# Optimization experiments

Hardware: AMD Instinct MI355X
Metric: run time of the kernel (lower is better)

The kernel has to match this reference:

```python
import jax, jax.numpy as jnp
import numpy as np

IN_CHANNELS = 128
N_NODES = 100000
N_EDGES = 625000


def setup_inputs() -> dict:
    key = jax.random.key(0)
    k1, k2, k3, k4, k5, k6 = jax.random.split(key, 6)
    d = IN_CHANNELS
    x = jax.random.normal(k1, (N_NODES, d), dtype=jnp.float32)
    edge_index = jax.random.randint(k2, (2, N_EDGES), 0, N_NODES, dtype=jnp.int64)
    # Linear params, torch default init: U(-1/sqrt(fan_in), 1/sqrt(fan_in))
    b1_bound = 1.0 / np.sqrt(2 * d)
    W1 = jax.random.uniform(k3, (d, 2 * d), minval=-b1_bound, maxval=b1_bound, dtype=jnp.float32)
    b1 = jax.random.uniform(k4, (d,), minval=-b1_bound, maxval=b1_bound, dtype=jnp.float32)
    b2_bound = 1.0 / np.sqrt(d)
    W2 = jax.random.uniform(k5, (1, d), minval=-b2_bound, maxval=b2_bound, dtype=jnp.float32)
    b2 = jax.random.uniform(k6, (1,), minval=-b2_bound, maxval=b2_bound, dtype=jnp.float32)
    return {"x": x, "edge_index": edge_index, "W1": W1, "b1": b1, "W2": W2, "b2": b2}


def reference(x, edge_index, W1, b1, W2, b2):
    # Gather endpoint features and concat along feature dim: [E, 2d]
    h = jnp.concatenate([x[edge_index[0]], x[edge_index[1]]], axis=1)
    h = jax.nn.relu(h @ W1.T + b1)          # [E, d]
    h = jax.nn.relu(h @ W2.T + b2)          # [E, 1]
    return jax.nn.sigmoid(h)
```

## Files before the change

kernel.cpp:

```cpp
#include <hip/hip_runtime.h>
#include <hip/hip_bf16.h>
#include <hip/hip_fp16.h>
#include <math.h>


typedef short    s16x4 __attribute__((ext_vector_type(4)));
typedef short    s16x8 __attribute__((ext_vector_type(8)));
typedef float    f32x4 __attribute__((ext_vector_type(4)));
typedef _Float16 h16x2 __attribute__((ext_vector_type(2)));
typedef _Float16 h16x8 __attribute__((ext_vector_type(8)));

#define D    128
#define CWLD 80

static __device__ inline short f2bf(float f) {
    unsigned u = __builtin_bit_cast(unsigned, f);
    unsigned r = (u + 0x7FFFu + ((u >> 16) & 1u)) >> 16;
    return (short)r;
}

static __device__ inline unsigned enc1_sw(float f) {
    f = fminf(fmaxf(f, -448.f), 448.f);
    unsigned short h = __builtin_bit_cast(unsigned short, (_Float16)(f * (1.0f / 256.0f)));
    unsigned s = (h >> 8) & 0x80u;
    unsigned mag = h & 0x7FFFu;
    mag = mag + 0x3Fu + ((mag >> 7) & 1u);
    return s | ((mag >> 7) & 0x7Fu);
}
static __device__ inline unsigned enc2(float a, float b) {
#if __has_builtin(__builtin_amdgcn_cvt_pk_fp8_f32)
    return ((unsigned)__builtin_amdgcn_cvt_pk_fp8_f32(a, b, 0, false)) & 0xFFFFu;
#else
    return enc1_sw(a) | (enc1_sw(b) << 8);
#endif
}

#if __has_builtin(__builtin_amdgcn_cvt_pk_f16_fp8)
#define YSC 1.0f
static __device__ inline h16x2 dec2lo(unsigned v) {
    return __builtin_amdgcn_cvt_pk_f16_fp8((short)v);
}
static __device__ inline h16x2 dec2hi(unsigned v) {
    return __builtin_amdgcn_cvt_pk_f16_fp8((short)(v >> 16));
}
#else
#define YSC 256.0f
static __device__ inline h16x2 dec2lo(unsigned v) {
    unsigned p = __builtin_amdgcn_perm(0u, v, 0x0C010C00u);
    unsigned h = ((p << 8) & 0x80008000u) | ((p << 7) & 0x3F803F80u);
    return __builtin_bit_cast(h16x2, h);
}
static __device__ inline h16x2 dec2hi(unsigned v) {
    unsigned p = __builtin_amdgcn_perm(0u, v, 0x0C030C02u);
    unsigned h = ((p << 8) & 0x80008000u) | ((p << 7) & 0x3F803F80u);
    return __builtin_bit_cast(h16x2, h);
}
#endif

static __device__ inline h16x2 reluh(h16x2 v) {
#if __has_builtin(__builtin_elementwise_max)
    h16x2 z = { (_Float16)0.0f, (_Float16)0.0f };
    return __builtin_elementwise_max(v, z);
#else
    unsigned u = __builtin_bit_cast(unsigned, v);
    unsigned m = ((u >> 15) & 0x00010001u) * 0xFFFFu;
    u &= ~m;
    return __builtin_bit_cast(h16x2, u);
#endif
}

static __device__ inline float dot2acc(h16x2 a, h16x2 b, float c) {
#if __has_builtin(__builtin_amdgcn_fdot2)
    return __builtin_amdgcn_fdot2(a, b, c, false);
#else
    return c + (float)a[0] * (float)b[0] + (float)a[1] * (float)b[1];
#endif
}

__global__ __launch_bounds__(256) void pack_w1_kernel(
    const float* __restrict__ W1, short* __restrict__ W1F)
{
    int g    = blockIdx.x * 256 + threadIdx.x;
    int lane = g & 63;
    int c    = (g >> 6) & 3;
    int j    = (g >> 8) & 3;
    int cs   = g >> 10;
    int o    = cs * 64 + j * 16 + (lane & 15);
    int kb   = c * 32 + (lane >> 4) * 8;
    const float* wp = W1 + (size_t)(o & 127) * 256 + (o >> 7) * 128 + kb;
    float4 u0 = *(const float4*)wp;
    float4 u1 = *(const float4*)(wp + 4);
    s16x8 v = { f2bf(u0.x), f2bf(u0.y), f2bf(u0.z), f2bf(u0.w),
                f2bf(u1.x), f2bf(u1.y), f2bf(u1.z), f2bf(u1.w) };
    *(s16x8*)&W1F[(size_t)g * 8] = v;
}

__global__ __launch_bounds__(64) void precompute_kernel(
    const float* __restrict__ x,
    const short* __restrict__ W1F,
    const float* __restrict__ b1,
    unsigned char* __restrict__ Y8,
    int N)
{
    __shared__ _Float16 Cw[32 * CWLD];

    const int lane = threadIdx.x;
    const int quad = lane >> 4, l15 = lane & 15;
    const int cs   = blockIdx.x;
    const int m0   = blockIdx.y * 32;

    float4 ar[2][4][2];
    #pragma unroll
    for (int i = 0; i < 2; ++i) {
        int m = m0 + i * 16 + l15; if (m >= N) m = N - 1;
        const float* xp = &x[(size_t)m * D + quad * 8];
        #pragma unroll
        for (int c = 0; c < 4; ++c) {
            ar[i][c][0] = *(const float4*)(xp + c * 32);
            ar[i][c][1] = *(const float4*)(xp + c * 32 + 4);
        }
    }

    s16x8 bf[4][4];
    #pragma unroll
    for (int j = 0; j < 4; ++j)
        #pragma unroll
        for (int c = 0; c < 4; ++c)
            bf[c][j] = *(const s16x8*)&W1F[(size_t)(((cs * 4 + j) * 4 + c) * 64 + lane) * 8];

    f32x4 acc[2][4] = {};
    #pragma unroll
    for (int c = 0; c < 4; ++c) {
        s16x8 af[2];
        #pragma unroll
        for (int i = 0; i < 2; ++i)
            af[i] = (s16x8){ f2bf(ar[i][c][0].x), f2bf(ar[i][c][0].y),
                             f2bf(ar[i][c][0].z), f2bf(ar[i][c][0].w),
                             f2bf(ar[i][c][1].x), f2bf(ar[i][c][1].y),
                             f2bf(ar[i][c][1].z), f2bf(ar[i][c][1].w) };
        #pragma unroll
        for (int i = 0; i < 2; ++i)
            #pragma unroll
            for (int j = 0; j < 4; ++j)
                acc[i][j] = __builtin_amdgcn_mfma_f32_16x16x32_bf16(
                    af[i], bf[c][j], acc[i][j], 0, 0, 0);
    }

    float b1v[4];
    #pragma unroll
    for (int j = 0; j < 4; ++j)
        b1v[j] = (cs < 2) ? b1[cs * 64 + j * 16 + l15] : 0.f;

    #pragma unroll
    for (int i = 0; i < 2; ++i)
        #pragma unroll
        for (int j = 0; j < 4; ++j)
            #pragma unroll
            for (int r = 0; r < 4; ++r)
                Cw[(i * 16 + quad * 4 + r) * CWLD + j * 16 + l15] =
                    (_Float16)(acc[i][j][r] + b1v[j]);

    __syncthreads();

    #pragma unroll
    for (int p = 0; p < 2; ++p) {
        int row = p * 16 + (lane >> 2);
        int m   = m0 + row;
        if (m < N) {
            const _Float16* sp = &Cw[row * CWLD + (lane & 3) * 16];
            uint4 ov;
            unsigned dw[4];
            #pragma unroll
            for (int q = 0; q < 4; ++q)
                dw[q] = enc2((float)sp[q*4+0], (float)sp[q*4+1])
                      | (enc2((float)sp[q*4+2], (float)sp[q*4+3]) << 16);
            ov.x = dw[0]; ov.y = dw[1]; ov.z = dw[2]; ov.w = dw[3];
            *(uint4*)&Y8[(size_t)m * 256 + cs * 64 + (lane & 3) * 16] = ov;
        }
    }
}

#define EPB 128

__global__ __launch_bounds__(256) void edge_kernel(
    const unsigned char* __restrict__ Y8,
    const int*           __restrict__ ei,
    const float*         __restrict__ W2,
    const float*         __restrict__ b2,
    float*               __restrict__ out,
    int E)
{
    const int tid = threadIdx.x;
    const int sub = tid & 7;
    const int grp = tid >> 3;
    const int e0  = blockIdx.x * EPB + grp;

    h16x2 w2h[8];
    {
        const float* wp = &W2[sub * 16];
        #pragma unroll
        for (int q = 0; q < 8; ++q) {
            float2 f = *(const float2*)(wp + q * 2);
            w2h[q] = (h16x2){ (_Float16)(f.x * YSC), (_Float16)(f.y * YSC) };
        }
    }

    int  ee[4]; bool vv[4]; uint4 L[4], R[4];
    #pragma unroll
    for (int k = 0; k < 4; ++k) {
        ee[k] = e0 + 32 * k;
        vv[k] = (ee[k] < E);
        int src = vv[k] ? ei[ee[k]] : 0;
        int dst = vv[k] ? ei[E + ee[k]] : 0;
        L[k] = *(const uint4*)(Y8 + (size_t)src * 256 + sub * 16);
        R[k] = *(const uint4*)(Y8 + (size_t)dst * 256 + 128 + sub * 16);
    }

    float s[4] = { 0.f, 0.f, 0.f, 0.f };
    #pragma unroll
    for (int k = 0; k < 4; ++k) {
        const unsigned* a = (const unsigned*)&L[k];
        const unsigned* c = (const unsigned*)&R[k];
        #pragma unroll
        for (int d = 0; d < 4; ++d) {
            h16x2 za = reluh(dec2lo(a[d]) + dec2lo(c[d]));
            s[k] = dot2acc(za, w2h[2*d],     s[k]);
            h16x2 zb = reluh(dec2hi(a[d]) + dec2hi(c[d]));
            s[k] = dot2acc(zb, w2h[2*d + 1], s[k]);
        }
    }

    #pragma unroll
    for (int k = 0; k < 4; ++k) {
        s[k] += __shfl_xor(s[k], 1);
        s[k] += __shfl_xor(s[k], 2);
        s[k] += __shfl_xor(s[k], 4);
    }

    if (sub == 0) {
        float bb = b2[0];
        #pragma unroll
        for (int k = 0; k < 4; ++k) {
            if (vv[k]) {
                float t = fmaxf(s[k] + bb, 0.f);
                out[ee[k]] = 1.0f / (1.0f + expf(-t));
            }
        }
    }
}

#define BM   128
#define BK   64
#define LDT  72

__global__ __launch_bounds__(256) void decoder_fallback_kernel(
    const float* __restrict__ x, const int* __restrict__ ei,
    const float* __restrict__ W1, const float* __restrict__ b1,
    const float* __restrict__ W2, const float* __restrict__ b2,
    float* __restrict__ out, int E)
{
    __shared__ int   nid[2][BM];
    __shared__ short At[BM * LDT];
    __shared__ short Bt[D * LDT];
    __shared__ float rowsum[BM][2];

    const int tid = threadIdx.x;
    const int e0  = blockIdx.x * BM;
    if (tid < BM) { int e = e0 + tid; nid[0][tid] = (e < E) ? ei[e] : 0; }
    else { int e = e0 + (tid - BM); nid[1][tid - BM] = (e < E) ? ei[E + e] : 0; }

    const int wid = tid >> 6, lane = tid & 63;
    const int wm = wid >> 1, wn = wid & 1;
    const int quad = lane >> 4, l15 = lane & 15;
    const int srow = tid >> 4, scol = (tid & 15) * 4;
    f32x4 acc[4][4] = {};
    __syncthreads();

    for (int t = 0; t < 4; ++t) {
        const int* ids = nid[t >> 1];
        const int kx = (t & 1) * BK, kw = t * BK;
        #pragma unroll
        for (int p = 0; p < 8; ++p) {
            int row = srow + p * 16;
            float4 v = *(const float4*)&x[(size_t)ids[row] * D + kx + scol];
            s16x4 bv = { f2bf(v.x), f2bf(v.y), f2bf(v.z), f2bf(v.w) };
            *(s16x4*)&At[row * LDT + scol] = bv;
        }
        #pragma unroll
        for (int p = 0; p < 8; ++p) {
            int n = srow + p * 16;
            float4 v = *(const float4*)&W1[n * 256 + kw + scol];
            s16x4 bv = { f2bf(v.x), f2bf(v.y), f2bf(v.z), f2bf(v.w) };
            *(s16x4*)&Bt[n * LDT + scol] = bv;
        }
        __syncthreads();
        #pragma unroll
        for (int c = 0; c < 2; ++c) {
            const int kc = c * 32;
            s16x8 af[4], bfr[4];
            #pragma unroll
            for (int i = 0; i < 4; ++i)
                af[i] = *(const s16x8*)&At[(wm*64 + i*16 + l15) * LDT + kc + quad*8];
            #pragma unroll
            for (int j = 0; j < 4; ++j)
                bfr[j] = *(const s16x8*)&Bt[(wn*64 + j*16 + l15) * LDT + kc + quad*8];
            #pragma unroll
            for (int i = 0; i < 4; ++i)
                #pragma unroll
                for (int j = 0; j < 4; ++j)
                    acc[i][j] = __builtin_amdgcn_mfma_f32_16x16x32_bf16(
                        af[i], bfr[j], acc[i][j], 0, 0, 0);
        }
        __syncthreads();
    }
    float b1v[4], w2v[4];
    #pragma unroll
    for (int j = 0; j < 4; ++j) {
        int col = wn*64 + j*16 + l15;
        b1v[j] = b1[col]; w2v[j] = W2[col];
    }
    float psum[16];
    #pragma unroll
    for (int t = 0; t < 16; ++t) psum[t] = 0.f;
    #pragma unroll
    for (int i = 0; i < 4; ++i)
        #pragma unroll
        for (int j = 0; j < 4; ++j)
            #pragma unroll
            for (int r = 0; r < 4; ++r) {
                float c = fmaxf(acc[i][j][r] + b1v[j], 0.f);
                psum[i*4 + r] += c * w2v[j];
            }
    #pragma unroll
    for (int off = 1; off < 16; off <<= 1)
        #pragma unroll
        for (int t = 0; t < 16; ++t)
            psum[t] += __shfl_xor(psum[t], off);
    if (l15 == 0) {
        #pragma unroll
        for (int i = 0; i < 4; ++i)
            #pragma unroll
            for (int r = 0; r < 4; ++r)
                rowsum[wm*64 + i*16 + quad*4 + r][wn] = psum[i*4 + r];
    }
    __syncthreads();
    if (tid < BM) {
        int e = e0 + tid;
        if (e < E) {
            float s = rowsum[tid][0] + rowsum[tid][1] + b2[0];
            s = fmaxf(s, 0.f);
            out[e] = 1.0f / (1.0f + expf(-s));
        }
    }
}

extern "C" void kernel_launch(void* const* d_in, const int* in_sizes, int n_in,
                              void* d_out, int out_size, void* d_ws, size_t ws_size,
                              hipStream_t stream) {
    const float* x  = (const float*)d_in[0];
    const int*   ei = (const int*)d_in[1];
    const float* W1 = (const float*)d_in[2];
    const float* b1 = (const float*)d_in[3];
    const float* W2 = (const float*)d_in[4];
    const float* b2 = (const float*)d_in[5];
    float* out = (float*)d_out;

    int E = in_sizes[1] / 2;
    int N = in_sizes[0] / D;

    size_t y_bytes = (size_t)N * 256;
    size_t need    = y_bytes + 32768 * sizeof(short);
    if (ws_size >= need) {
        unsigned char* Y8  = (unsigned char*)d_ws;
        short*         W1F = (short*)((char*)d_ws + y_bytes);
        pack_w1_kernel<<<16, 256, 0, stream>>>(W1, W1F);
        dim3 gridA(4, (N + 31) / 32);
        precompute_kernel<<<gridA, 64, 0, stream>>>(x, W1F, b1, Y8, N);
        int gridB = (E + EPB - 1) / EPB;
        edge_kernel<<<gridB, 256, 0, stream>>>(Y8, ei, W2, b2, out, E);
    } else {
        int nblocks = (E + BM - 1) / BM;
        decoder_fallback_kernel<<<nblocks, 256, 0, stream>>>(
            x, ei, W1, b1, W2, b2, out, E);
    }
}
```

Baseline: 151.8 us.

## Share x tile across four column-slice waves via LDS in precompute kernel

The precompute kernel now launches one 256-thread block per 32-row tile, with four waves each handling one 64-column output slice. Previously four separate 64-thread blocks each loaded and converted the same x rows. The x tile is loaded once cooperatively, converted to bf16 into shared memory, and read back as MFMA A-fragments. This cuts redundant global reads of x and repeated f32-to-bf16 conversion by four times, at the cost of an extra barrier, more LDS per block and fewer blocks.

```diff
diff --git a/kernel.cpp b/kernel.cpp
--- a/kernel.cpp
+++ b/kernel.cpp
@@ -11,6 +11,7 @@
 typedef _Float16 h16x8 __attribute__((ext_vector_type(8)));
 
 #define D    128
+#define ALD  136
 #define CWLD 80
 
 static __device__ inline short f2bf(float f) {
@@ -95,30 +96,32 @@
     *(s16x8*)&W1F[(size_t)g * 8] = v;
 }
 
-__global__ __launch_bounds__(64) void precompute_kernel(
+__global__ __launch_bounds__(256) void precompute_kernel(
     const float* __restrict__ x,
     const short* __restrict__ W1F,
     const float* __restrict__ b1,
     unsigned char* __restrict__ Y8,
     int N)
 {
-    __shared__ _Float16 Cw[32 * CWLD];
-
-    const int lane = threadIdx.x;
+    __shared__ short    At[32 * ALD];
+    __shared__ _Float16 Cw[4][32 * CWLD];
+
+    const int tid  = threadIdx.x;
+    const int wid  = tid >> 6;
+    const int lane = tid & 63;
     const int quad = lane >> 4, l15 = lane & 15;
-    const int cs   = blockIdx.x;
-    const int m0   = blockIdx.y * 32;
-
-    float4 ar[2][4][2];
-    #pragma unroll
-    for (int i = 0; i < 2; ++i) {
-        int m = m0 + i * 16 + l15; if (m >= N) m = N - 1;
-        const float* xp = &x[(size_t)m * D + quad * 8];
-        #pragma unroll
-        for (int c = 0; c < 4; ++c) {
-            ar[i][c][0] = *(const float4*)(xp + c * 32);
-            ar[i][c][1] = *(const float4*)(xp + c * 32 + 4);
-        }
+    const int m0   = blockIdx.x * 32;
+    const int cs   = wid;
+
+    const int srow = tid >> 3;
+    const int sc0  = (tid & 7) * 4;
+    float4 xv[4];
+    {
+        int m = m0 + srow; if (m >= N) m = N - 1;
+        const float* xp = &x[(size_t)m * D + sc0];
+        #pragma unroll
+        for (int p = 0; p < 4; ++p)
+            xv[p] = *(const float4*)(xp + p * 32);
     }
 
     s16x8 bf[4][4];
@@ -128,16 +131,21 @@
         for (int c = 0; c < 4; ++c)
             bf[c][j] = *(const s16x8*)&W1F[(size_t)(((cs * 4 + j) * 4 + c) * 64 + lane) * 8];
 
+    #pragma unroll
+    for (int p = 0; p < 4; ++p) {
+        s16x4 bv = { f2bf(xv[p].x), f2bf(xv[p].y), f2bf(xv[p].z), f2bf(xv[p].w) };
+        *(s16x4*)&At[srow * ALD + sc0 + p * 32] = bv;
+    }
+    __syncthreads();
+
     f32x4 acc[2][4] = {};
     #pragma unroll
     for (int c = 0; c < 4; ++c) {
+        const int kc = c * 32;
         s16x8 af[2];
         #pragma unroll
         for (int i = 0; i < 2; ++i)
-            af[i] = (s16x8){ f2bf(ar[i][c][0].x), f2bf(ar[i][c][0].y),
-                             f2bf(ar[i][c][0].z), f2bf(ar[i][c][0].w),
-                             f2bf(ar[i][c][1].x), f2bf(ar[i][c][1].y),
-                             f2bf(ar[i][c][1].z), f2bf(ar[i][c][1].w) };
+            af[i] = *(const s16x8*)&At[(i * 16 + l15) * ALD + kc + quad * 8];
         #pragma unroll
         for (int i = 0; i < 2; ++i)
             #pragma unroll
@@ -151,13 +159,14 @@
     for (int j = 0; j < 4; ++j)
         b1v[j] = (cs < 2) ? b1[cs * 64 + j * 16 + l15] : 0.f;
 
+    _Float16* cw = &Cw[wid][0];
     #pragma unroll
     for (int i = 0; i < 2; ++i)
         #pragma unroll
         for (int j = 0; j < 4; ++j)
             #pragma unroll
             for (int r = 0; r < 4; ++r)
-                Cw[(i * 16 + quad * 4 + r) * CWLD + j * 16 + l15] =
+                cw[(i * 16 + quad * 4 + r) * CWLD + j * 16 + l15] =
                     (_Float16)(acc[i][j][r] + b1v[j]);
 
     __syncthreads();
@@ -167,7 +176,7 @@
         int row = p * 16 + (lane >> 2);
         int m   = m0 + row;
         if (m < N) {
-            const _Float16* sp = &Cw[row * CWLD + (lane & 3) * 16];
+            const _Float16* sp = &cw[row * CWLD + (lane & 3) * 16];
             uint4 ov;
             unsigned dw[4];
             #pragma unroll
@@ -374,8 +383,8 @@
         unsigned char* Y8  = (unsigned char*)d_ws;
         short*         W1F = (short*)((char*)d_ws + y_bytes);
         pack_w1_kernel<<<16, 256, 0, stream>>>(W1, W1F);
-        dim3 gridA(4, (N + 31) / 32);
-        precompute_kernel<<<gridA, 64, 0, stream>>>(x, W1F, b1, Y8, N);
+        int gridA = (N + 31) / 32;
+        precompute_kernel<<<gridA, 256, 0, stream>>>(x, W1F, b1, Y8, N);
         int gridB = (E + EPB - 1) / EPB;
         edge_kernel<<<gridB, 256, 0, stream>>>(Y8, ei, W2, b2, out, E);
     } else {
```

Measured after the change: 133.7 us. 11.9% less time.
